# Kernel optimization log

Hardware: AMD Instinct MI355X
Metric: run time of the kernel (lower is better)

## Reference

```python
import jax, jax.numpy as jnp
import numpy as np
from jax import lax

# Shared Conv2d [1,1] + BN + ReLU is represented as a per-point affine (BN folded
# into conv weight/bias at eval) followed by ReLU, matching inference-mode math.

B, N1, N2, K = 8, 8192, 2048, 8
C1, C2 = 64, 128
MLP0, MLP1, MLP2 = 128, 128, 128  # mlp=[128,128], mlp2=[128]


def setup_inputs() -> dict:
    key = jax.random.key(0)
    ks = jax.random.split(key, 10)
    sc = lambda fan_in: 1.0 / np.sqrt(fan_in)
    return {
        "xyz1": jax.random.normal(ks[0], (B, N1, 3), jnp.float32),
        "xyz2": jax.random.normal(ks[1], (B, N2, 3), jnp.float32),
        "feat1": jax.random.normal(ks[2], (B, N1, C1), jnp.float32),
        "feat2": jax.random.normal(ks[3], (B, N2, C2), jnp.float32),
        "W0": jax.random.normal(ks[4], (C2 + 3, MLP0), jnp.float32) * sc(C2 + 3),
        "b0": jnp.zeros((MLP0,), jnp.float32),
        "W1": jax.random.normal(ks[5], (MLP0, MLP1), jnp.float32) * sc(MLP0),
        "b1": jnp.zeros((MLP1,), jnp.float32),
        "W2": jax.random.normal(ks[6], (MLP1 + C1, MLP2), jnp.float32) * sc(MLP1 + C1),
        "b2": jnp.zeros((MLP2,), jnp.float32),
    }


def _knn_idx(xyz1, xyz2, k):
    # squared distances (B, N1, N2); top-k nearest in xyz2 for each xyz1 point
    d2 = jnp.sum((xyz1[:, :, None, :] - xyz2[:, None, :, :]) ** 2, axis=-1)
    _, idx = lax.top_k(-d2, k)  # (B, N1, K)
    return idx


def _gather(src, idx):
    # src: (B, N2, C), idx: (B, N1, K) -> (B, N1, K, C)
    return jax.vmap(lambda s, i: s[i])(src, idx)


def reference(xyz1, xyz2, feat1, feat2, W0, b0, W1, b1, W2, b2):
    idx = _knn_idx(xyz1, xyz2, K)
    xyz2_g = _gather(xyz2, idx)            # (B, N1, K, 3)
    feat2_g = _gather(feat2, idx)          # (B, N1, K, C2)
    xyz_diff = xyz2_g - xyz1[:, :, None, :]
    net = jnp.concatenate([feat2_g, xyz_diff], axis=-1)  # (B, N1, K, C2+3)
    net = jax.nn.relu(net @ W0 + b0)
    net = jax.nn.relu(net @ W1 + b1)       # (B, N1, K, MLP1)
    pooled = jnp.max(net, axis=2)          # max pooling over neighbors
    cat = jnp.concatenate([pooled, feat1], axis=-1)      # (B, N1, MLP1+C1)
    out = jax.nn.relu(cat @ W2 + b2)       # (B, N1, MLP2)
    return out
```

## Files before the change

kernel.cpp:

```cpp
#include <hip/hip_runtime.h>
#include <hip/hip_bf16.h>

constexpr int B_  = 8;
constexpr int N1_ = 8192;
constexpr int N2_ = 2048;
constexpr int K_  = 8;

typedef short bf16x8 __attribute__((ext_vector_type(8)));
typedef float f32x4  __attribute__((ext_vector_type(4)));
typedef float f32x2  __attribute__((ext_vector_type(2)));

__device__ __forceinline__ short f2b(float x) {
    __hip_bfloat16 h = __float2bfloat16(x);
    return *reinterpret_cast<short*>(&h);
}

#define CASF(a, b) { const float _lo = fminf(a, b); \
                     const float _hi = fmaxf(a, b); \
                     (a) = _lo; (b) = _hi; }

__global__ __launch_bounds__(256) void prep_all(
    const float* __restrict__ feat2, short* __restrict__ feat2b,
    const float* __restrict__ W0, const float* __restrict__ W1,
    const float* __restrict__ W2, const float* __restrict__ xyz2,
    short* __restrict__ W0T, short* __restrict__ W1T, short* __restrict__ W2T,
    float* __restrict__ xp) {
    if (blockIdx.x < 2048) {
        const int i = blockIdx.x * 256 + threadIdx.x;
        const float4 v = ((const float4*)feat2)[i];
        uint2 o;
        o.x = (unsigned short)f2b(v.x) | ((unsigned)(unsigned short)f2b(v.y) << 16);
        o.y = (unsigned short)f2b(v.z) | ((unsigned)(unsigned short)f2b(v.w) << 16);
        ((uint2*)feat2b)[i] = o;
        return;
    }
    int i = (blockIdx.x - 2048) * 256 + threadIdx.x;
    if (i < 128 * 160) {
        const int n = i / 160, k = i % 160;
        W0T[i] = (k < 131) ? f2b(W0[k * 128 + n]) : (short)0;
        return;
    }
    i -= 128 * 160;
    if (i < 128 * 128) {
        const int n = i >> 7, k = i & 127;
        W1T[i] = f2b(W1[k * 128 + n]);
        return;
    }
    i -= 128 * 128;
    if (i < 128 * 192) {
        const int n = i / 192, k = i % 192;
        W2T[i] = f2b(W2[k * 128 + n]);
        return;
    }
    i -= 128 * 192;
    const int b = i >> 11, j = i & 2047;
    const float* src = xyz2 + ((size_t)b * N2_ + j) * 3;
    float* dst = xp + (size_t)b * 3 * N2_ + j;
    dst[0]        = src[0];
    dst[N2_]      = src[1];
    dst[2 * N2_]  = src[2];
}

constexpr int LCAP = 76;

__global__ __launch_bounds__(256) void knn_lazy(const float* __restrict__ xyz1,
                                                const float* __restrict__ xp,
                                                int* __restrict__ idx) {
    __shared__ __align__(16) unsigned short sMem[78 * 256];
    float* sD = (float*)sMem;
    int*   sI = (int*)sMem + 64 * 33;

    const int b = blockIdx.y;
    const int lane = threadIdx.x & 63;
    const int s = threadIdx.x >> 6;
    const int tid = threadIdx.x;
    const int n = blockIdx.x * 64 + lane;

    const float* q = xyz1 + ((size_t)b * N1_ + n) * 3;
    const float qx = q[0], qy = q[1], qz = q[2];
    const float* xs = xp + (size_t)b * 3 * N2_ + s * 512;
    const float* ys = xs + N2_;
    const float* zs = xs + 2 * N2_;

    float bd[K_];
#pragma unroll
    for (int t = 0; t < K_; ++t) bd[t] = 3.0e38f;
    int cnt = 0;

    const f32x2 qx2 = {qx, qx}, qy2 = {qy, qy}, qz2 = {qz, qz};

    for (int j0 = 0; j0 < 512; j0 += 8) {
        const float4 X0 = *(const float4*)(xs + j0);
        const float4 X1 = *(const float4*)(xs + j0 + 4);
        const float4 Y0 = *(const float4*)(ys + j0);
        const float4 Y1 = *(const float4*)(ys + j0 + 4);
        const float4 Z0 = *(const float4*)(zs + j0);
        const float4 Z1 = *(const float4*)(zs + j0 + 4);
        float xf[8];
        {
            f32x2 dx, dy, dz, d;
            dx = qx2 - f32x2{X0.x, X0.y}; dy = qy2 - f32x2{Y0.x, Y0.y}; dz = qz2 - f32x2{Z0.x, Z0.y};
            d = dx * dx + dy * dy + dz * dz; xf[0] = d.x; xf[1] = d.y;
            dx = qx2 - f32x2{X0.z, X0.w}; dy = qy2 - f32x2{Y0.z, Y0.w}; dz = qz2 - f32x2{Z0.z, Z0.w};
            d = dx * dx + dy * dy + dz * dz; xf[2] = d.x; xf[3] = d.y;
            dx = qx2 - f32x2{X1.x, X1.y}; dy = qy2 - f32x2{Y1.x, Y1.y}; dz = qz2 - f32x2{Z1.x, Z1.y};
            d = dx * dx + dy * dy + dz * dz; xf[4] = d.x; xf[5] = d.y;
            dx = qx2 - f32x2{X1.z, X1.w}; dy = qy2 - f32x2{Y1.z, Y1.w}; dz = qz2 - f32x2{Z1.z, Z1.w};
            d = dx * dx + dy * dy + dz * dz; xf[6] = d.x; xf[7] = d.y;
        }
        const float thr = bd[K_ - 1] * 1.0000038f;
#pragma unroll
        for (int u = 0; u < 8; ++u) {
            const bool acc = xf[u] < thr;
            if (acc) {
                const int capped = cnt < LCAP ? cnt : LCAP;
                sMem[capped * 256 + tid] = (unsigned short)(j0 + u);
                cnt++;
            }
        }
        CASF(xf[0], xf[1]); CASF(xf[2], xf[3]); CASF(xf[4], xf[5]); CASF(xf[6], xf[7]);
        CASF(xf[0], xf[2]); CASF(xf[1], xf[3]); CASF(xf[4], xf[6]); CASF(xf[5], xf[7]);
        CASF(xf[1], xf[2]); CASF(xf[5], xf[6]); CASF(xf[0], xf[4]); CASF(xf[3], xf[7]);
        CASF(xf[1], xf[5]); CASF(xf[2], xf[6]);
        CASF(xf[1], xf[4]); CASF(xf[3], xf[6]);
        CASF(xf[2], xf[4]); CASF(xf[3], xf[5]);
        CASF(xf[3], xf[4]);
        float t0 = fminf(bd[0], xf[7]);
        float t1 = fminf(bd[1], xf[6]);
        float t2 = fminf(bd[2], xf[5]);
        float t3 = fminf(bd[3], xf[4]);
        float t4 = fminf(bd[4], xf[3]);
        float t5 = fminf(bd[5], xf[2]);
        float t6 = fminf(bd[6], xf[1]);
        float t7 = fminf(bd[7], xf[0]);
        CASF(t0, t4); CASF(t1, t5); CASF(t2, t6); CASF(t3, t7);
        CASF(t0, t2); CASF(t1, t3); CASF(t4, t6); CASF(t5, t7);
        CASF(t0, t1); CASF(t2, t3); CASF(t4, t5); CASF(t6, t7);
        bd[0] = t0; bd[1] = t1; bd[2] = t2; bd[3] = t3;
        bd[4] = t4; bd[5] = t5; bd[6] = t6; bd[7] = t7;
    }

    float rd[K_];
    int   ri[K_];
#pragma unroll
    for (int t = 0; t < K_; ++t) { rd[t] = 3.0e38f; ri[t] = 0; }
    const int m = cnt < LCAP ? cnt : LCAP;
    for (int t = 0;; ++t) {
        const bool act = t < m;
        if (!__any(act)) break;
        if (act) {
#pragma clang fp contract(off)
            const int jl = sMem[t * 256 + tid];
            const float dx = qx - xs[jl];
            const float dy = qy - ys[jl];
            const float dz = qz - zs[jl];
            const float dx2 = dx * dx;
            const float dy2 = dy * dy;
            const float dz2 = dz * dz;
            const float d2 = (dx2 + dy2) + dz2;
            if (d2 < rd[K_ - 1]) {
                rd[K_ - 1] = d2; ri[K_ - 1] = s * 512 + jl;
#pragma unroll
                for (int t2 = K_ - 1; t2 >= 1; --t2) {
                    if (rd[t2] < rd[t2 - 1]) {
                        float td = rd[t2]; rd[t2] = rd[t2 - 1]; rd[t2 - 1] = td;
                        int   ti = ri[t2]; ri[t2] = ri[t2 - 1]; ri[t2 - 1] = ti;
                    }
                }
            }
        }
    }

    if (__any(cnt > LCAP)) {
        if (cnt > LCAP) {
#pragma unroll
            for (int t = 0; t < K_; ++t) { rd[t] = 3.0e38f; ri[t] = 0; }
            for (int j = 0; j < 512; ++j) {
#pragma clang fp contract(off)
                const float dx = qx - xs[j];
                const float dy = qy - ys[j];
                const float dz = qz - zs[j];
                const float dx2 = dx * dx;
                const float dy2 = dy * dy;
                const float dz2 = dz * dz;
                const float d2 = (dx2 + dy2) + dz2;
                if (d2 < rd[K_ - 1]) {
                    rd[K_ - 1] = d2; ri[K_ - 1] = s * 512 + j;
#pragma unroll
                    for (int t2 = K_ - 1; t2 >= 1; --t2) {
                        if (rd[t2] < rd[t2 - 1]) {
                            float td = rd[t2]; rd[t2] = rd[t2 - 1]; rd[t2 - 1] = td;
                            int   ti = ri[t2]; ri[t2] = ri[t2 - 1]; ri[t2 - 1] = ti;
                        }
                    }
                }
            }
        }
    }

    __syncthreads();
#pragma unroll
    for (int t = 0; t < K_; ++t) {
        sD[lane * 33 + s * 8 + t] = rd[t];
        sI[lane * 33 + s * 8 + t] = ri[t];
    }
    __syncthreads();

    if (tid < 64) {
        const int qq = tid;
        int h[4] = {0, 0, 0, 0};
        const int base = (b * N1_ + n) * K_;
#pragma unroll
        for (int t = 0; t < K_; ++t) {
            float best = 3.1e38f;
            int   bidx = 0, bs = 0;
#pragma unroll
            for (int ss = 0; ss < 4; ++ss) {
                if (h[ss] < 8) {
                    const float d = sD[qq * 33 + ss * 8 + h[ss]];
                    if (d < best) { best = d; bidx = sI[qq * 33 + ss * 8 + h[ss]]; bs = ss; }
                }
            }
#pragma unroll
            for (int ss = 0; ss < 4; ++ss) h[ss] += (ss == bs) ? 1 : 0;
            idx[base + t] = bidx;
        }
    }
}

__global__ __launch_bounds__(256) void fused_mfma(
    const float* __restrict__ xyz1, const float* __restrict__ xyz2,
    const float* __restrict__ feat1,
    const float* __restrict__ b0, const float* __restrict__ b1,
    const float* __restrict__ b2,
    const short* __restrict__ feat2b, const short* __restrict__ W0T,
    const short* __restrict__ W1T, const short* __restrict__ W2T,
    const int* __restrict__ idx, float* __restrict__ out) {
    __shared__ __align__(16) short sA[128 * 168];
    __shared__ __align__(16) short sCat[16 * 200];

    const int bid = blockIdx.x;
    const int b = bid & 7;
    const int n0 = (bid >> 3) * 16;
    const int tid = threadIdx.x;

    {
        const int row = tid >> 1, half = tid & 1;
        const int p = row >> 3, kk = row & 7;
        const int n = n0 + p;
        const int j = idx[((size_t)b * N1_ + n) * K_ + kk];
        const uint4* src = (const uint4*)(feat2b + ((size_t)(b * N2_ + j)) * 128 + half * 64);
        uint4* dst = (uint4*)(sA + row * 168 + half * 64);
#pragma unroll
        for (int t = 0; t < 8; ++t) dst[t] = src[t];
        uint4* pad = (uint4*)(sA + row * 168 + 128 + half * 16);
        if (half == 0) {
            const float dx = xyz2[((size_t)b * N2_ + j) * 3 + 0] - xyz1[((size_t)b * N1_ + n) * 3 + 0];
            const float dy = xyz2[((size_t)b * N2_ + j) * 3 + 1] - xyz1[((size_t)b * N1_ + n) * 3 + 1];
            const float dz = xyz2[((size_t)b * N2_ + j) * 3 + 2] - xyz1[((size_t)b * N1_ + n) * 3 + 2];
            uint4 v;
            v.x = (unsigned short)f2b(dx) | ((unsigned)(unsigned short)f2b(dy) << 16);
            v.y = (unsigned short)f2b(dz);
            v.z = 0; v.w = 0;
            pad[0] = v;
            pad[1] = make_uint4(0, 0, 0, 0);
        } else {
            pad[0] = make_uint4(0, 0, 0, 0);
            pad[1] = make_uint4(0, 0, 0, 0);
        }
    }
    {
#pragma unroll
        for (int u = 0; u < 4; ++u) {
            const int e = tid * 4 + u;
            const int p = e >> 6, c = e & 63;
            sCat[p * 200 + 128 + c] = f2b(feat1[((size_t)b * N1_ + n0 + p) * 64 + c]);
        }
    }
    __syncthreads();

    const int wave = tid >> 6, lane = tid & 63;
    const int q = lane >> 4, l15 = lane & 15;
    const int mBase = (wave & 1) * 64, nBase = (wave >> 1) * 64;

    const f32x4 zero4 = {0.f, 0.f, 0.f, 0.f};

    f32x4 acc[4][4];
#pragma unroll
    for (int mt = 0; mt < 4; ++mt)
#pragma unroll
        for (int nt = 0; nt < 4; ++nt) acc[mt][nt] = zero4;

    for (int ks = 0; ks < 5; ++ks) {
        bf16x8 af[4], bf[4];
#pragma unroll
        for (int mt = 0; mt < 4; ++mt)
            af[mt] = *(const bf16x8*)(sA + (mBase + mt * 16 + l15) * 168 + ks * 32 + q * 8);
#pragma unroll
        for (int nt = 0; nt < 4; ++nt)
            bf[nt] = *(const bf16x8*)(W0T + (nBase + nt * 16 + l15) * 160 + ks * 32 + q * 8);
#pragma unroll
        for (int mt = 0; mt < 4; ++mt)
#pragma unroll
            for (int nt = 0; nt < 4; ++nt)
                acc[mt][nt] = __builtin_amdgcn_mfma_f32_16x16x32_bf16(af[mt], bf[nt], acc[mt][nt], 0, 0, 0);
    }

    float b0v[4];
#pragma unroll
    for (int nt = 0; nt < 4; ++nt) b0v[nt] = b0[nBase + nt * 16 + l15];
    __syncthreads();
#pragma unroll
    for (int mt = 0; mt < 4; ++mt)
#pragma unroll
        for (int nt = 0; nt < 4; ++nt)
#pragma unroll
            for (int r = 0; r < 4; ++r) {
                const int row = mBase + mt * 16 + q * 4 + r;
                const int col = nBase + nt * 16 + l15;
                sA[row * 136 + col] = f2b(fmaxf(acc[mt][nt][r] + b0v[nt], 0.0f));
            }
    __syncthreads();

    f32x4 acc2[4][4];
#pragma unroll
    for (int mt = 0; mt < 4; ++mt)
#pragma unroll
        for (int nt = 0; nt < 4; ++nt) acc2[mt][nt] = zero4;

    for (int ks = 0; ks < 4; ++ks) {
        bf16x8 af[4], bf[4];
#pragma unroll
        for (int mt = 0; mt < 4; ++mt)
            af[mt] = *(const bf16x8*)(sA + (mBase + mt * 16 + l15) * 136 + ks * 32 + q * 8);
#pragma unroll
        for (int nt = 0; nt < 4; ++nt)
            bf[nt] = *(const bf16x8*)(W1T + (nBase + nt * 16 + l15) * 128 + ks * 32 + q * 8);
#pragma unroll
        for (int mt = 0; mt < 4; ++mt)
#pragma unroll
            for (int nt = 0; nt < 4; ++nt)
                acc2[mt][nt] = __builtin_amdgcn_mfma_f32_16x16x32_bf16(af[mt], bf[nt], acc2[mt][nt], 0, 0, 0);
    }

    float b1v[4];
#pragma unroll
    for (int nt = 0; nt < 4; ++nt) b1v[nt] = b1[nBase + nt * 16 + l15];
#pragma unroll
    for (int mt = 0; mt < 4; ++mt)
#pragma unroll
        for (int nt = 0; nt < 4; ++nt) {
            float vm = fmaxf(acc2[mt][nt][0] + b1v[nt], 0.0f);
#pragma unroll
            for (int r = 1; r < 4; ++r) vm = fmaxf(vm, acc2[mt][nt][r] + b1v[nt]);
            const float other = __shfl_xor(vm, 16);
            const float pool = fmaxf(vm, other);
            if ((q & 1) == 0) {
                const int pp = (mBase >> 3) + mt * 2 + (q >> 1);
                sCat[pp * 200 + nBase + nt * 16 + l15] = f2b(pool);
            }
        }
    __syncthreads();

    f32x4 acc3[2];
    acc3[0] = zero4; acc3[1] = zero4;
    const int nB2 = wave * 32;
    for (int ks = 0; ks < 6; ++ks) {
        const bf16x8 a2 = *(const bf16x8*)(sCat + l15 * 200 + ks * 32 + q * 8);
#pragma unroll
        for (int nt = 0; nt < 2; ++nt) {
            const bf16x8 b2f = *(const bf16x8*)(W2T + (nB2 + nt * 16 + l15) * 192 + ks * 32 + q * 8);
            acc3[nt] = __builtin_amdgcn_mfma_f32_16x16x32_bf16(a2, b2f, acc3[nt], 0, 0, 0);
        }
    }
    float b2v[2];
#pragma unroll
    for (int nt = 0; nt < 2; ++nt) b2v[nt] = b2[nB2 + nt * 16 + l15];
#pragma unroll
    for (int nt = 0; nt < 2; ++nt)
#pragma unroll
        for (int r = 0; r < 4; ++r) {
            const int p = q * 4 + r;
            const int col = nB2 + nt * 16 + l15;
            out[((size_t)(b * N1_ + n0 + p)) * 128 + col] = fmaxf(acc3[nt][r] + b2v[nt], 0.0f);
        }
}

extern "C" void kernel_launch(void* const* d_in, const int* in_sizes, int n_in,
                              void* d_out, int out_size, void* d_ws, size_t ws_size,
                              hipStream_t stream) {
    const float* xyz1  = (const float*)d_in[0];
    const float* xyz2  = (const float*)d_in[1];
    const float* feat1 = (const float*)d_in[2];
    const float* feat2 = (const float*)d_in[3];
    const float* W0    = (const float*)d_in[4];
    const float* b0    = (const float*)d_in[5];
    const float* W1    = (const float*)d_in[6];
    const float* b1    = (const float*)d_in[7];
    const float* W2    = (const float*)d_in[8];
    const float* b2    = (const float*)d_in[9];
    float* out = (float*)d_out;

    char* ws = (char*)d_ws;
    int*    idx    = (int*)(ws + 0);
    short*  feat2b = (short*)(ws + 2097152);
    short*  W0T    = (short*)(ws + 6291456);
    short*  W1T    = (short*)(ws + 6332416);
    short*  W2T    = (short*)(ws + 6365184);
    float*  xp     = (float*)(ws + 6414336);

    prep_all<<<2352, 256, 0, stream>>>(feat2, feat2b, W0, W1, W2, xyz2,
                                       W0T, W1T, W2T, xp);
    knn_lazy<<<dim3(N1_ / 64, B_), 256, 0, stream>>>(xyz1, xp, idx);
    fused_mfma<<<dim3(8 * (N1_ / 16)), 256, 0, stream>>>(xyz1, xyz2, feat1, b0, b1, b2,
                                                         feat2b, W0T, W1T, W2T, idx, out);
}
```

Before: 314.0 us.

## Give each wave full-width row slabs and shrink LDS in fused MLP kernel

The fused MLP kernel is repartitioned so each wave owns 32 gathered rows across all 128 output columns instead of a 64x64 quadrant. Each wave now consumes only rows it wrote itself, so the barriers between the first and second matmul stages are dropped. The xyz-difference features are built directly in registers and applied as a separate MFMA K-step, which removes the padded 168-wide LDS rows. The concat buffer is aliased onto the same LDS array and launch bounds request 4 blocks per CU, aiming for higher occupancy. In exchange, each wave now loads the full W0/W1 fragments from global memory, and the 4-blocks-per-CU bound may force register spills.

```diff
diff --git a/kernel.cpp b/kernel.cpp
--- a/kernel.cpp
+++ b/kernel.cpp
@@ -228,7 +228,7 @@
     }
 }
 
-__global__ __launch_bounds__(256) void fused_mfma(
+__global__ __launch_bounds__(256, 4) void fused_mfma(
     const float* __restrict__ xyz1, const float* __restrict__ xyz2,
     const float* __restrict__ feat1,
     const float* __restrict__ b0, const float* __restrict__ b1,
@@ -236,135 +236,154 @@
     const short* __restrict__ feat2b, const short* __restrict__ W0T,
     const short* __restrict__ W1T, const short* __restrict__ W2T,
     const int* __restrict__ idx, float* __restrict__ out) {
-    __shared__ __align__(16) short sA[128 * 168];
-    __shared__ __align__(16) short sCat[16 * 200];
+    __shared__ __align__(16) short sA[128 * 136];
+    short* sCat = sA;
 
     const int bid = blockIdx.x;
     const int b = bid & 7;
     const int n0 = (bid >> 3) * 16;
     const int tid = threadIdx.x;
+    const int w = tid >> 6;
+    const int lane = tid & 63;
+    const int q = lane >> 4, l15 = lane & 15;
+    const int rowBase = w * 32;
 
     {
-        const int row = tid >> 1, half = tid & 1;
+        const int row = rowBase + (lane >> 1);
+        const int half = lane & 1;
         const int p = row >> 3, kk = row & 7;
         const int n = n0 + p;
         const int j = idx[((size_t)b * N1_ + n) * K_ + kk];
         const uint4* src = (const uint4*)(feat2b + ((size_t)(b * N2_ + j)) * 128 + half * 64);
-        uint4* dst = (uint4*)(sA + row * 168 + half * 64);
+        uint4* dst = (uint4*)(sA + row * 136 + half * 64);
 #pragma unroll
         for (int t = 0; t < 8; ++t) dst[t] = src[t];
-        uint4* pad = (uint4*)(sA + row * 168 + 128 + half * 16);
-        if (half == 0) {
-            const float dx = xyz2[((size_t)b * N2_ + j) * 3 + 0] - xyz1[((size_t)b * N1_ + n) * 3 + 0];
-            const float dy = xyz2[((size_t)b * N2_ + j) * 3 + 1] - xyz1[((size_t)b * N1_ + n) * 3 + 1];
-            const float dz = xyz2[((size_t)b * N2_ + j) * 3 + 2] - xyz1[((size_t)b * N1_ + n) * 3 + 2];
-            uint4 v;
-            v.x = (unsigned short)f2b(dx) | ((unsigned)(unsigned short)f2b(dy) << 16);
-            v.y = (unsigned short)f2b(dz);
-            v.z = 0; v.w = 0;
-            pad[0] = v;
-            pad[1] = make_uint4(0, 0, 0, 0);
-        } else {
-            pad[0] = make_uint4(0, 0, 0, 0);
-            pad[1] = make_uint4(0, 0, 0, 0);
-        }
-    }
-    {
-#pragma unroll
-        for (int u = 0; u < 4; ++u) {
-            const int e = tid * 4 + u;
-            const int p = e >> 6, c = e & 63;
-            sCat[p * 200 + 128 + c] = f2b(feat1[((size_t)b * N1_ + n0 + p) * 64 + c]);
-        }
-    }
+    }
+    bf16x8 af4[2];
+#pragma unroll
+    for (int mt = 0; mt < 2; ++mt) {
+        const int row = rowBase + mt * 16 + l15;
+        const int p = row >> 3, kk = row & 7;
+        const int n = n0 + p;
+        const int j = idx[((size_t)b * N1_ + n) * K_ + kk];
+        const float dx = xyz2[((size_t)b * N2_ + j) * 3 + 0] - xyz1[((size_t)b * N1_ + n) * 3 + 0];
+        const float dy = xyz2[((size_t)b * N2_ + j) * 3 + 1] - xyz1[((size_t)b * N1_ + n) * 3 + 1];
+        const float dz = xyz2[((size_t)b * N2_ + j) * 3 + 2] - xyz1[((size_t)b * N1_ + n) * 3 + 2];
+        bf16x8 v = {0, 0, 0, 0, 0, 0, 0, 0};
+        if (q == 0) { v[0] = f2b(dx); v[1] = f2b(dy); v[2] = f2b(dz); }
+        af4[mt] = v;
+    }
+
+    const f32x4 zero4 = {0.f, 0.f, 0.f, 0.f};
+
+    f32x4 acc[2][8];
+#pragma unroll
+    for (int mt = 0; mt < 2; ++mt)
+#pragma unroll
+        for (int nt = 0; nt < 8; ++nt) acc[mt][nt] = zero4;
+
+    for (int ks = 0; ks < 4; ++ks) {
+        bf16x8 af[2];
+#pragma unroll
+        for (int mt = 0; mt < 2; ++mt)
+            af[mt] = *(const bf16x8*)(sA + (rowBase + mt * 16 + l15) * 136 + ks * 32 + q * 8);
+#pragma unroll
+        for (int h = 0; h < 2; ++h) {
+            bf16x8 bf[4];
+#pragma unroll
+            for (int nt = 0; nt < 4; ++nt)
+                bf[nt] = *(const bf16x8*)(W0T + ((h * 4 + nt) * 16 + l15) * 160 + ks * 32 + q * 8);
+#pragma unroll
+            for (int mt = 0; mt < 2; ++mt)
+#pragma unroll
+                for (int nt = 0; nt < 4; ++nt)
+                    acc[mt][h * 4 + nt] = __builtin_amdgcn_mfma_f32_16x16x32_bf16(af[mt], bf[nt], acc[mt][h * 4 + nt], 0, 0, 0);
+        }
+    }
+#pragma unroll
+    for (int h = 0; h < 2; ++h) {
+        bf16x8 bf[4];
+#pragma unroll
+        for (int nt = 0; nt < 4; ++nt)
+            bf[nt] = *(const bf16x8*)(W0T + ((h * 4 + nt) * 16 + l15) * 160 + 128 + q * 8);
+#pragma unroll
+        for (int mt = 0; mt < 2; ++mt)
+#pragma unroll
+            for (int nt = 0; nt < 4; ++nt)
+                acc[mt][h * 4 + nt] = __builtin_amdgcn_mfma_f32_16x16x32_bf16(af4[mt], bf[nt], acc[mt][h * 4 + nt], 0, 0, 0);
+    }
+
+    float b0v[8];
+#pragma unroll
+    for (int nt = 0; nt < 8; ++nt) b0v[nt] = b0[nt * 16 + l15];
+#pragma unroll
+    for (int mt = 0; mt < 2; ++mt)
+#pragma unroll
+        for (int nt = 0; nt < 8; ++nt)
+#pragma unroll
+            for (int r = 0; r < 4; ++r) {
+                const int row = rowBase + mt * 16 + q * 4 + r;
+                const int col = nt * 16 + l15;
+                sA[row * 136 + col] = f2b(fmaxf(acc[mt][nt][r] + b0v[nt], 0.0f));
+            }
+
+    f32x4 acc2[2][8];
+#pragma unroll
+    for (int mt = 0; mt < 2; ++mt)
+#pragma unroll
+        for (int nt = 0; nt < 8; ++nt) acc2[mt][nt] = zero4;
+
+    for (int ks = 0; ks < 4; ++ks) {
+        bf16x8 af[2];
+#pragma unroll
+        for (int mt = 0; mt < 2; ++mt)
+            af[mt] = *(const bf16x8*)(sA + (rowBase + mt * 16 + l15) * 136 + ks * 32 + q * 8);
+#pragma unroll
+        for (int h = 0; h < 2; ++h) {
+            bf16x8 bf[4];
+#pragma unroll
+            for (int nt = 0; nt < 4; ++nt)
+                bf[nt] = *(const bf16x8*)(W1T + ((h * 4 + nt) * 16 + l15) * 128 + ks * 32 + q * 8);
+#pragma unroll
+            for (int mt = 0; mt < 2; ++mt)
+#pragma unroll
+                for (int nt = 0; nt < 4; ++nt)
+                    acc2[mt][h * 4 + nt] = __builtin_amdgcn_mfma_f32_16x16x32_bf16(af[mt], bf[nt], acc2[mt][h * 4 + nt], 0, 0, 0);
+        }
+    }
+
+    float b1v[8];
+#pragma unroll
+    for (int nt = 0; nt < 8; ++nt) b1v[nt] = b1[nt * 16 + l15];
+
     __syncthreads();
 
-    const int wave = tid >> 6, lane = tid & 63;
-    const int q = lane >> 4, l15 = lane & 15;
-    const int mBase = (wave & 1) * 64, nBase = (wave >> 1) * 64;
-
-    const f32x4 zero4 = {0.f, 0.f, 0.f, 0.f};
-
-    f32x4 acc[4][4];
-#pragma unroll
-    for (int mt = 0; mt < 4; ++mt)
-#pragma unroll
-        for (int nt = 0; nt < 4; ++nt) acc[mt][nt] = zero4;
-
-    for (int ks = 0; ks < 5; ++ks) {
-        bf16x8 af[4], bf[4];
-#pragma unroll
-        for (int mt = 0; mt < 4; ++mt)
-            af[mt] = *(const bf16x8*)(sA + (mBase + mt * 16 + l15) * 168 + ks * 32 + q * 8);
-#pragma unroll
-        for (int nt = 0; nt < 4; ++nt)
-            bf[nt] = *(const bf16x8*)(W0T + (nBase + nt * 16 + l15) * 160 + ks * 32 + q * 8);
-#pragma unroll
-        for (int mt = 0; mt < 4; ++mt)
-#pragma unroll
-            for (int nt = 0; nt < 4; ++nt)
-                acc[mt][nt] = __builtin_amdgcn_mfma_f32_16x16x32_bf16(af[mt], bf[nt], acc[mt][nt], 0, 0, 0);
-    }
-
-    float b0v[4];
-#pragma unroll
-    for (int nt = 0; nt < 4; ++nt) b0v[nt] = b0[nBase + nt * 16 + l15];
-    __syncthreads();
-#pragma unroll
-    for (int mt = 0; mt < 4; ++mt)
-#pragma unroll
-        for (int nt = 0; nt < 4; ++nt)
-#pragma unroll
-            for (int r = 0; r < 4; ++r) {
-                const int row = mBase + mt * 16 + q * 4 + r;
-                const int col = nBase + nt * 16 + l15;
-                sA[row * 136 + col] = f2b(fmaxf(acc[mt][nt][r] + b0v[nt], 0.0f));
-            }
-    __syncthreads();
-
-    f32x4 acc2[4][4];
-#pragma unroll
-    for (int mt = 0; mt < 4; ++mt)
-#pragma unroll
-        for (int nt = 0; nt < 4; ++nt) acc2[mt][nt] = zero4;
-
-    for (int ks = 0; ks < 4; ++ks) {
-        bf16x8 af[4], bf[4];
-#pragma unroll
-        for (int mt = 0; mt < 4; ++mt)
-            af[mt] = *(const bf16x8*)(sA + (mBase + mt * 16 + l15) * 136 + ks * 32 + q * 8);
-#pragma unroll
-        for (int nt = 0; nt < 4; ++nt)
-            bf[nt] = *(const bf16x8*)(W1T + (nBase + nt * 16 + l15) * 128 + ks * 32 + q * 8);
-#pragma unroll
-        for (int mt = 0; mt < 4; ++mt)
-#pragma unroll
-            for (int nt = 0; nt < 4; ++nt)
-                acc2[mt][nt] = __builtin_amdgcn_mfma_f32_16x16x32_bf16(af[mt], bf[nt], acc2[mt][nt], 0, 0, 0);
-    }
-
-    float b1v[4];
-#pragma unroll
-    for (int nt = 0; nt < 4; ++nt) b1v[nt] = b1[nBase + nt * 16 + l15];
-#pragma unroll
-    for (int mt = 0; mt < 4; ++mt)
-#pragma unroll
-        for (int nt = 0; nt < 4; ++nt) {
+#pragma unroll
+    for (int mt = 0; mt < 2; ++mt)
+#pragma unroll
+        for (int nt = 0; nt < 8; ++nt) {
             float vm = fmaxf(acc2[mt][nt][0] + b1v[nt], 0.0f);
 #pragma unroll
             for (int r = 1; r < 4; ++r) vm = fmaxf(vm, acc2[mt][nt][r] + b1v[nt]);
             const float other = __shfl_xor(vm, 16);
             const float pool = fmaxf(vm, other);
             if ((q & 1) == 0) {
-                const int pp = (mBase >> 3) + mt * 2 + (q >> 1);
-                sCat[pp * 200 + nBase + nt * 16 + l15] = f2b(pool);
-            }
-        }
+                const int pp = w * 4 + mt * 2 + (q >> 1);
+                sCat[pp * 200 + nt * 16 + l15] = f2b(pool);
+            }
+        }
+    {
+        const int p = w * 4 + (lane >> 4);
+        const int c4 = l15 * 4;
+        const float4 f4 = *(const float4*)(feat1 + ((size_t)b * N1_ + n0 + p) * 64 + c4);
+        short* d = sCat + p * 200 + 128 + c4;
+        d[0] = f2b(f4.x); d[1] = f2b(f4.y); d[2] = f2b(f4.z); d[3] = f2b(f4.w);
+    }
     __syncthreads();
 
     f32x4 acc3[2];
     acc3[0] = zero4; acc3[1] = zero4;
-    const int nB2 = wave * 32;
+    const int nB2 = w * 32;
     for (int ks = 0; ks < 6; ++ks) {
         const bf16x8 a2 = *(const bf16x8*)(sCat + l15 * 200 + ks * 32 + q * 8);
 #pragma unroll
```

Result: slower. 355.3 us (+13.2%).

## Shrink LDS footprint by aliasing sCat onto sA and compacting xyz tile

Applied to the files above, without the earlier changes.

Cuts the per-block shared-memory allocation by removing the padded 168-wide rows and storing the xyz-difference columns in a separate compact 8-wide buffer. sCat now aliases sA, which needs an extra barrier before it is reused. The feat1 tile is loaded early as one float4 per thread and written to LDS after pooling. This replaces the strided scalar loads. A launch-bounds hint of 4 blocks per CU targets higher occupancy, at the risk of register pressure or spills from the 64-element accumulator tile.

```diff
diff --git a/kernel.cpp b/kernel.cpp
--- a/kernel.cpp
+++ b/kernel.cpp
@@ -228,7 +228,7 @@
     }
 }
 
-__global__ __launch_bounds__(256) void fused_mfma(
+__global__ __launch_bounds__(256, 4) void fused_mfma(
     const float* __restrict__ xyz1, const float* __restrict__ xyz2,
     const float* __restrict__ feat1,
     const float* __restrict__ b0, const float* __restrict__ b1,
@@ -236,13 +236,16 @@
     const short* __restrict__ feat2b, const short* __restrict__ W0T,
     const short* __restrict__ W1T, const short* __restrict__ W2T,
     const int* __restrict__ idx, float* __restrict__ out) {
-    __shared__ __align__(16) short sA[128 * 168];
-    __shared__ __align__(16) short sCat[16 * 200];
+    __shared__ __align__(16) short sA[128 * 136 + 128 * 8];
+    short* sXyz = sA + 128 * 136;
+    short* sCat = sA;
 
     const int bid = blockIdx.x;
     const int b = bid & 7;
     const int n0 = (bid >> 3) * 16;
     const int tid = threadIdx.x;
+
+    const float4 f1v = *(const float4*)(feat1 + ((size_t)b * N1_ + n0 + (tid >> 4)) * 64 + (tid & 15) * 4);
 
     {
         const int row = tid >> 1, half = tid & 1;
@@ -250,10 +253,9 @@
         const int n = n0 + p;
         const int j = idx[((size_t)b * N1_ + n) * K_ + kk];
         const uint4* src = (const uint4*)(feat2b + ((size_t)(b * N2_ + j)) * 128 + half * 64);
-        uint4* dst = (uint4*)(sA + row * 168 + half * 64);
+        uint4* dst = (uint4*)(sA + row * 136 + half * 64);
 #pragma unroll
         for (int t = 0; t < 8; ++t) dst[t] = src[t];
-        uint4* pad = (uint4*)(sA + row * 168 + 128 + half * 16);
         if (half == 0) {
             const float dx = xyz2[((size_t)b * N2_ + j) * 3 + 0] - xyz1[((size_t)b * N1_ + n) * 3 + 0];
             const float dy = xyz2[((size_t)b * N2_ + j) * 3 + 1] - xyz1[((size_t)b * N1_ + n) * 3 + 1];
@@ -262,19 +264,7 @@
             v.x = (unsigned short)f2b(dx) | ((unsigned)(unsigned short)f2b(dy) << 16);
             v.y = (unsigned short)f2b(dz);
             v.z = 0; v.w = 0;
-            pad[0] = v;
-            pad[1] = make_uint4(0, 0, 0, 0);
-        } else {
-            pad[0] = make_uint4(0, 0, 0, 0);
-            pad[1] = make_uint4(0, 0, 0, 0);
-        }
-    }
-    {
-#pragma unroll
-        for (int u = 0; u < 4; ++u) {
-            const int e = tid * 4 + u;
-            const int p = e >> 6, c = e & 63;
-            sCat[p * 200 + 128 + c] = f2b(feat1[((size_t)b * N1_ + n0 + p) * 64 + c]);
+            *(uint4*)(sXyz + row * 8) = v;
         }
     }
     __syncthreads();
@@ -291,14 +281,28 @@
 #pragma unroll
         for (int nt = 0; nt < 4; ++nt) acc[mt][nt] = zero4;
 
-    for (int ks = 0; ks < 5; ++ks) {
+    for (int ks = 0; ks < 4; ++ks) {
         bf16x8 af[4], bf[4];
 #pragma unroll
         for (int mt = 0; mt < 4; ++mt)
-            af[mt] = *(const bf16x8*)(sA + (mBase + mt * 16 + l15) * 168 + ks * 32 + q * 8);
+            af[mt] = *(const bf16x8*)(sA + (mBase + mt * 16 + l15) * 136 + ks * 32 + q * 8);
 #pragma unroll
         for (int nt = 0; nt < 4; ++nt)
             bf[nt] = *(const bf16x8*)(W0T + (nBase + nt * 16 + l15) * 160 + ks * 32 + q * 8);
+#pragma unroll
+        for (int mt = 0; mt < 4; ++mt)
+#pragma unroll
+            for (int nt = 0; nt < 4; ++nt)
+                acc[mt][nt] = __builtin_amdgcn_mfma_f32_16x16x32_bf16(af[mt], bf[nt], acc[mt][nt], 0, 0, 0);
+    }
+    {
+        bf16x8 af[4], bf[4];
+#pragma unroll
+        for (int mt = 0; mt < 4; ++mt)
+            af[mt] = *(const bf16x8*)(sXyz + (mBase + mt * 16 + l15) * 8);
+#pragma unroll
+        for (int nt = 0; nt < 4; ++nt)
+            bf[nt] = *(const bf16x8*)(W0T + (nBase + nt * 16 + l15) * 160 + 128 + q * 8);
 #pragma unroll
         for (int mt = 0; mt < 4; ++mt)
 #pragma unroll
@@ -346,6 +350,9 @@
     float b1v[4];
 #pragma unroll
     for (int nt = 0; nt < 4; ++nt) b1v[nt] = b1[nBase + nt * 16 + l15];
+
+    __syncthreads();
+
 #pragma unroll
     for (int mt = 0; mt < 4; ++mt)
 #pragma unroll
@@ -360,6 +367,14 @@
                 sCat[pp * 200 + nBase + nt * 16 + l15] = f2b(pool);
             }
         }
+    {
+        const int p = tid >> 4;
+        const int c4 = (tid & 15) * 4;
+        uint2 w;
+        w.x = (unsigned short)f2b(f1v.x) | ((unsigned)(unsigned short)f2b(f1v.y) << 16);
+        w.y = (unsigned short)f2b(f1v.z) | ((unsigned)(unsigned short)f2b(f1v.w) << 16);
+        *(uint2*)(sCat + p * 200 + 128 + c4) = w;
+    }
     __syncthreads();
 
     f32x4 acc3[2];
```

Measured after the change: 312.2 us. About the same (-0.6%).
